# Kernel optimization log

Measured on AMD Instinct MI355X. Metric: run time of the kernel, lower is better.

## Reference

```python
import jax, jax.numpy as jnp
import numpy as np

B, N, E = 2, 4096, 256
H, TAU = 8, 32
HD = E // H
SCALING = HD ** -0.5


def setup_inputs() -> dict:
    key0 = jax.random.key(0)
    kq, kk, kv, kw = jax.random.split(key0, 4)
    return {
        "query": jax.random.normal(kq, (B, N, E), dtype=jnp.float32),
        "key": jax.random.normal(kk, (B, N, E), dtype=jnp.float32),
        "value": jax.random.normal(kv, (B, N, E), dtype=jnp.float32),
        "W": jax.random.normal(kw, (E, E), dtype=jnp.float32) * 0.02,
        "b": jnp.zeros((E,), dtype=jnp.float32),
    }


def reference(query, key, value, W, b):
    b_, n_, e_ = query.shape
    # Zero-pad the front so token i attends to keys/values at positions
    # [i - TAU + 1, ..., i] (sliding causal window of length TAU).
    pad = jnp.zeros((b_, TAU - 1, e_), dtype=query.dtype)
    kp = jnp.concatenate([pad, key], axis=1)   # [B, N+TAU-1, E]
    vp = jnp.concatenate([pad, value], axis=1)
    win_idx = jnp.arange(n_)[:, None] + jnp.arange(TAU)[None, :]  # [N, TAU]
    wk = kp[:, win_idx]  # [B, N, TAU, E] (materialized windows, as torch unfold does)
    wv = vp[:, win_idx]

    proj = lambda x: x @ W.T + b  # shared projection for q, k, v (single nn.Linear)
    q = proj(query).reshape(b_, n_, H, HD)            # [B, N, H, HD]
    k = proj(wk).reshape(b_, n_, TAU, H, HD)          # [B, N, TAU, H, HD]
    v = proj(wv).reshape(b_, n_, TAU, H, HD)

    scores = jnp.einsum("bnhd,bnthd->bhnt", q, k) * SCALING  # [B, H, N, TAU]
    attn = jax.nn.softmax(scores, axis=-1)
    out = jnp.einsum("bhnt,bnthd->bnhd", attn, v)             # [B, N, H, HD]
    return out.reshape(b_, n_, e_)
```

## Files before the change

### kernel.cpp

```cpp
#include <hip/hip_runtime.h>

#define SCALING 0.17677669529663687f

typedef __attribute__((ext_vector_type(8))) short bf8;
typedef __attribute__((ext_vector_type(4))) short bf4;
typedef _Float16 half8 __attribute__((ext_vector_type(8)));
typedef _Float16 half4 __attribute__((ext_vector_type(4)));
typedef __attribute__((ext_vector_type(4))) float floatx4;

__device__ __forceinline__ short f2bf(float f) {
    union { float f; unsigned u; } v; v.f = f;
    unsigned u = v.u;
    return (short)((u + 0x7FFFu + ((u >> 16) & 1u)) >> 16);
}

#define PSTR 264
#define VSTR 72

__global__ __launch_bounds__(512, 2) void fused_kernel(
    const float* __restrict__ q, const float* __restrict__ k,
    const float* __restrict__ v, const float* __restrict__ W,
    const float* __restrict__ bias, float* __restrict__ out)
{
    __shared__ short    Pl[96][PSTR];
    __shared__ _Float16 Vt[256][VSTR];
    __shared__ _Float16 Ps[8][32][VSTR];
    __shared__ short    As[160][40];
    __shared__ short    Bs[256][40];

    const int tid = threadIdx.x;
    const int n0  = blockIdx.x * 32;
    const int b   = blockIdx.y;
    const int lane = tid & 63, wid = tid >> 6;
    const int wm = wid & 1, wn = wid >> 1;
    const int quad = lane >> 4, l16 = lane & 15;

    int a_row[3]; int a_c4[3]; const float* a_ptr[3];
    #pragma unroll
    for (int i = 0; i < 3; i++) {
        int idx = tid + i * 512;
        if (idx < 1280) {
            int r = idx >> 3;
            a_row[i] = r;
            a_c4[i]  = (idx & 7) * 4;
            const float* p;
            if (r < 32) {
                p = q + (size_t)(b * 4096 + n0 + r) * 256;
            } else if (r < 96) {
                int j = n0 + r - 64;
                p = (j >= 0) ? (k + (size_t)(b * 4096 + j) * 256) : nullptr;
            } else {
                int j = n0 + r - 128;
                p = (j >= 0) ? (v + (size_t)(b * 4096 + j) * 256) : nullptr;
            }
            a_ptr[i] = p;
        } else { a_row[i] = -1; a_c4[i] = 0; a_ptr[i] = nullptr; }
    }
    int w_row[4], w_c4[4];
    #pragma unroll
    for (int i = 0; i < 4; i++) {
        int idx = tid + i * 512;
        w_row[i] = idx >> 3;
        w_c4[i]  = (idx & 7) * 4;
    }

    floatx4 acc[5][4];
    #pragma unroll
    for (int mt = 0; mt < 5; mt++)
        #pragma unroll
        for (int nt = 0; nt < 4; nt++) acc[mt][nt] = (floatx4)0.0f;

    for (int k0 = 0; k0 < 256; k0 += 32) {
        bf4 ab[3];
        #pragma unroll
        for (int i = 0; i < 3; i++) {
            float4 xa = make_float4(0.f, 0.f, 0.f, 0.f);
            if (a_ptr[i]) xa = *(const float4*)(a_ptr[i] + k0 + a_c4[i]);
            ab[i][0] = f2bf(xa.x); ab[i][1] = f2bf(xa.y);
            ab[i][2] = f2bf(xa.z); ab[i][3] = f2bf(xa.w);
        }
        bf4 wb[4];
        #pragma unroll
        for (int i = 0; i < 4; i++) {
            float4 wv = *(const float4*)(W + (size_t)w_row[i] * 256 + k0 + w_c4[i]);
            wb[i][0] = f2bf(wv.x); wb[i][1] = f2bf(wv.y);
            wb[i][2] = f2bf(wv.z); wb[i][3] = f2bf(wv.w);
        }
        __syncthreads();
        #pragma unroll
        for (int i = 0; i < 3; i++)
            if (a_row[i] >= 0) *(bf4*)&As[a_row[i]][a_c4[i]] = ab[i];
        #pragma unroll
        for (int i = 0; i < 4; i++)
            *(bf4*)&Bs[w_row[i]][w_c4[i]] = wb[i];
        __syncthreads();

        bf8 af[5], bfr[4];
        #pragma unroll
        for (int mt = 0; mt < 5; mt++)
            af[mt] = *(const bf8*)&As[wm * 80 + mt * 16 + l16][quad * 8];
        #pragma unroll
        for (int nt = 0; nt < 4; nt++)
            bfr[nt] = *(const bf8*)&Bs[wn * 64 + nt * 16 + l16][quad * 8];
        #pragma unroll
        for (int mt = 0; mt < 5; mt++)
            #pragma unroll
            for (int nt = 0; nt < 4; nt++)
                acc[mt][nt] = __builtin_amdgcn_mfma_f32_16x16x32_bf16(
                    af[mt], bfr[nt], acc[mt][nt], 0, 0, 0);
    }

    #pragma unroll
    for (int nt = 0; nt < 4; nt++) {
        int col = wn * 64 + nt * 16 + l16;
        float bv = bias[col];
        #pragma unroll
        for (int mt = 0; mt < 5; mt++) {
            int rb = wm * 80 + mt * 16 + quad * 4;
            if (rb < 96) {
                const bool isQ = (rb < 32);
                #pragma unroll
                for (int r = 0; r < 4; r++) {
                    float val = acc[mt][nt][r] + bv;
                    Pl[rb + r][col] = f2bf(isQ ? val * SCALING : val);
                }
            } else {
                half4 hv;
                #pragma unroll
                for (int r = 0; r < 4; r++) hv[r] = (_Float16)(acc[mt][nt][r] + bv);
                *(half4*)&Vt[col][rb - 96] = hv;
            }
        }
    }
    __syncthreads();

    const int h  = wid;
    const int cb = h * 32;

    bf8 qf[2], kf[4];
    #pragma unroll
    for (int mt = 0; mt < 2; mt++)
        qf[mt] = *(const bf8*)&Pl[mt * 16 + l16][cb + quad * 8];
    #pragma unroll
    for (int jt = 0; jt < 4; jt++)
        kf[jt] = *(const bf8*)&Pl[32 + jt * 16 + l16][cb + quad * 8];

    floatx4 S[2][4];
    S[0][0] = __builtin_amdgcn_mfma_f32_16x16x32_bf16(qf[0], kf[0], (floatx4)0.f, 0, 0, 0);
    S[0][1] = __builtin_amdgcn_mfma_f32_16x16x32_bf16(qf[0], kf[1], (floatx4)0.f, 0, 0, 0);
    S[0][2] = __builtin_amdgcn_mfma_f32_16x16x32_bf16(qf[0], kf[2], (floatx4)0.f, 0, 0, 0);
    S[1][1] = __builtin_amdgcn_mfma_f32_16x16x32_bf16(qf[1], kf[1], (floatx4)0.f, 0, 0, 0);
    S[1][2] = __builtin_amdgcn_mfma_f32_16x16x32_bf16(qf[1], kf[2], (floatx4)0.f, 0, 0, 0);
    S[1][3] = __builtin_amdgcn_mfma_f32_16x16x32_bf16(qf[1], kf[3], (floatx4)0.f, 0, 0, 0);

    float p[2][3][4], inv[2][4];
    #pragma unroll
    for (int mt = 0; mt < 2; mt++) {
        #pragma unroll
        for (int r = 0; r < 4; r++) {
            int n = mt * 16 + quad * 4 + r;
            float sv[3], mx = -3.0e38f;
            #pragma unroll
            for (int u = 0; u < 3; u++) {
                int i = (u + mt) * 16 + l16;
                bool valid = (i > n) && (i <= n + 32);
                sv[u] = valid ? S[mt][u + mt][r] : -3.0e38f;
                mx = fmaxf(mx, sv[u]);
            }
            #pragma unroll
            for (int off = 1; off < 16; off <<= 1)
                mx = fmaxf(mx, __shfl_xor(mx, off, 64));
            float lsum = 0.f;
            #pragma unroll
            for (int u = 0; u < 3; u++) {
                float pv = (sv[u] > -1.0e38f) ? __expf(sv[u] - mx) : 0.f;
                p[mt][u][r] = pv;
                lsum += pv;
            }
            #pragma unroll
            for (int off = 1; off < 16; off <<= 1)
                lsum += __shfl_xor(lsum, off, 64);
            inv[mt][r] = 1.0f / lsum;
        }
    }

    _Float16 (*myPs)[VSTR] = Ps[h];
    #pragma unroll
    for (int mt = 0; mt < 2; mt++) {
        int zjt = (mt == 0) ? 3 : 0;
        #pragma unroll
        for (int r = 0; r < 4; r++) {
            int row = mt * 16 + quad * 4 + r;
            #pragma unroll
            for (int u = 0; u < 3; u++)
                myPs[row][(u + mt) * 16 + l16] = (_Float16)p[mt][u][r];
            myPs[row][zjt * 16 + l16] = (_Float16)0.f;
        }
    }

    half8 pf[2][2], vf[2][2];
    #pragma unroll
    for (int mt = 0; mt < 2; mt++)
        #pragma unroll
        for (int ks = 0; ks < 2; ks++)
            pf[mt][ks] = *(const half8*)&myPs[mt * 16 + l16][ks * 32 + quad * 8];
    #pragma unroll
    for (int dt = 0; dt < 2; dt++)
        #pragma unroll
        for (int ks = 0; ks < 2; ks++)
            vf[dt][ks] = *(const half8*)&Vt[cb + dt * 16 + l16][ks * 32 + quad * 8];

    floatx4 O[2][2];
    #pragma unroll
    for (int mt = 0; mt < 2; mt++)
        #pragma unroll
        for (int dt = 0; dt < 2; dt++) {
            O[mt][dt] = (floatx4)0.f;
            #pragma unroll
            for (int ks = 0; ks < 2; ks++)
                O[mt][dt] = __builtin_amdgcn_mfma_f32_16x16x32_f16(
                    pf[mt][ks], vf[dt][ks], O[mt][dt], 0, 0, 0);
        }

    const size_t obase = ((size_t)b * 4096 + n0) * 256;
    #pragma unroll
    for (int mt = 0; mt < 2; mt++)
        #pragma unroll
        for (int dt = 0; dt < 2; dt++)
            #pragma unroll
            for (int r = 0; r < 4; r++) {
                int n = mt * 16 + quad * 4 + r;
                out[obase + (size_t)n * 256 + cb + dt * 16 + l16] =
                    O[mt][dt][r] * inv[mt][r];
            }
}

extern "C" void kernel_launch(void* const* d_in, const int* in_sizes, int n_in,
                              void* d_out, int out_size, void* d_ws, size_t ws_size,
                              hipStream_t stream) {
    (void)in_sizes; (void)n_in; (void)out_size; (void)d_ws; (void)ws_size;
    const float* q    = (const float*)d_in[0];
    const float* k    = (const float*)d_in[1];
    const float* v    = (const float*)d_in[2];
    const float* W    = (const float*)d_in[3];
    const float* bias = (const float*)d_in[4];
    float* outp = (float*)d_out;

    hipLaunchKernelGGL(fused_kernel, dim3(128, 2), dim3(512), 0, stream,
                       q, k, v, W, bias, outp);
}
```

Before: 92.42 us.

## Pre-convert W to bf16, double-buffer A tiles, load W fragments from global

Adds a small pre-kernel that converts W to bf16 once per call in workspace. The main kernel now reads W fragments straight from global memory into registers, dropping the Bs shared tile. It double-buffers the activation tile with register prefetch so only one barrier is needed per k-step, and uses the hardware v_cvt_pk_bf16_f32 instruction instead of manual rounding. It also swizzles the block index to change the order in which sequence chunks are scheduled. The costs are an extra kernel launch and uncoalesced per-lane global reads of W.

```diff
diff --git a/kernel.cpp b/kernel.cpp
--- a/kernel.cpp
+++ b/kernel.cpp
@@ -8,28 +8,44 @@
 typedef _Float16 half4 __attribute__((ext_vector_type(4)));
 typedef __attribute__((ext_vector_type(4))) float floatx4;
 
-__device__ __forceinline__ short f2bf(float f) {
-    union { float f; unsigned u; } v; v.f = f;
-    unsigned u = v.u;
-    return (short)((u + 0x7FFFu + ((u >> 16) & 1u)) >> 16);
+__device__ __forceinline__ int cvt_pk_bf16(float a, float b) {
+    int r;
+    asm("v_cvt_pk_bf16_f32 %0, %1, %2" : "=v"(r) : "v"(a), "v"(b));
+    return r;
+}
+__device__ __forceinline__ bf4 cvt4_bf(float4 x) {
+    union { int i[2]; bf4 v; } u;
+    u.i[0] = cvt_pk_bf16(x.x, x.y);
+    u.i[1] = cvt_pk_bf16(x.z, x.w);
+    return u.v;
+}
+__device__ __forceinline__ short f2bf_hw(float f) {
+    return (short)cvt_pk_bf16(f, f);
 }
 
 #define PSTR 264
 #define VSTR 72
 
+__global__ void prep_w_kernel(const float* __restrict__ W, short* __restrict__ Wb) {
+    int i = (blockIdx.x * 256 + threadIdx.x) * 4;
+    float4 w = *(const float4*)(W + i);
+    *(bf4*)(Wb + i) = cvt4_bf(w);
+}
+
 __global__ __launch_bounds__(512, 2) void fused_kernel(
     const float* __restrict__ q, const float* __restrict__ k,
-    const float* __restrict__ v, const float* __restrict__ W,
+    const float* __restrict__ v, const short* __restrict__ Wb,
     const float* __restrict__ bias, float* __restrict__ out)
 {
     __shared__ short    Pl[96][PSTR];
     __shared__ _Float16 Vt[256][VSTR];
     __shared__ _Float16 Ps[8][32][VSTR];
-    __shared__ short    As[160][40];
-    __shared__ short    Bs[256][40];
+    __shared__ short    As[2][160][40];
 
     const int tid = threadIdx.x;
-    const int n0  = blockIdx.x * 32;
+    const int bxr = blockIdx.x;
+    const int bx  = (bxr & 7) * 16 + (bxr >> 3);
+    const int n0  = bx * 32;
     const int b   = blockIdx.y;
     const int lane = tid & 63, wid = tid >> 6;
     const int wm = wid & 1, wn = wid >> 1;
@@ -56,13 +72,11 @@
             a_ptr[i] = p;
         } else { a_row[i] = -1; a_c4[i] = 0; a_ptr[i] = nullptr; }
     }
-    int w_row[4], w_c4[4];
-    #pragma unroll
-    for (int i = 0; i < 4; i++) {
-        int idx = tid + i * 512;
-        w_row[i] = idx >> 3;
-        w_c4[i]  = (idx & 7) * 4;
-    }
+
+    const short* wfp[4];
+    #pragma unroll
+    for (int nt = 0; nt < 4; nt++)
+        wfp[nt] = Wb + (size_t)(wn * 64 + nt * 16 + l16) * 256 + quad * 8;
 
     floatx4 acc[5][4];
     #pragma unroll
@@ -70,44 +84,61 @@
         #pragma unroll
         for (int nt = 0; nt < 4; nt++) acc[mt][nt] = (floatx4)0.0f;
 
-    for (int k0 = 0; k0 < 256; k0 += 32) {
-        bf4 ab[3];
-        #pragma unroll
-        for (int i = 0; i < 3; i++) {
-            float4 xa = make_float4(0.f, 0.f, 0.f, 0.f);
-            if (a_ptr[i]) xa = *(const float4*)(a_ptr[i] + k0 + a_c4[i]);
-            ab[i][0] = f2bf(xa.x); ab[i][1] = f2bf(xa.y);
-            ab[i][2] = f2bf(xa.z); ab[i][3] = f2bf(xa.w);
-        }
-        bf4 wb[4];
-        #pragma unroll
-        for (int i = 0; i < 4; i++) {
-            float4 wv = *(const float4*)(W + (size_t)w_row[i] * 256 + k0 + w_c4[i]);
-            wb[i][0] = f2bf(wv.x); wb[i][1] = f2bf(wv.y);
-            wb[i][2] = f2bf(wv.z); wb[i][3] = f2bf(wv.w);
-        }
+    float4 xain[3];
+    #pragma unroll
+    for (int i = 0; i < 3; i++) {
+        xain[i] = make_float4(0.f, 0.f, 0.f, 0.f);
+        if (a_ptr[i]) xain[i] = *(const float4*)(a_ptr[i] + a_c4[i]);
+    }
+    #pragma unroll
+    for (int i = 0; i < 3; i++) {
+        bf4 t = cvt4_bf(xain[i]);
+        if (a_row[i] >= 0) *(bf4*)&As[0][a_row[i]][a_c4[i]] = t;
+    }
+    #pragma unroll
+    for (int i = 0; i < 3; i++) {
+        float4 t = make_float4(0.f, 0.f, 0.f, 0.f);
+        if (a_ptr[i]) t = *(const float4*)(a_ptr[i] + 32 + a_c4[i]);
+        xain[i] = t;
+    }
+    bf8 wf_cur[4], wf_nxt[4];
+    #pragma unroll
+    for (int nt = 0; nt < 4; nt++)
+        wf_cur[nt] = *(const bf8*)(wfp[nt]);
+
+    for (int it = 0; it < 8; ++it) {
+        const int cur = it & 1;
         __syncthreads();
-        #pragma unroll
-        for (int i = 0; i < 3; i++)
-            if (a_row[i] >= 0) *(bf4*)&As[a_row[i]][a_c4[i]] = ab[i];
-        #pragma unroll
-        for (int i = 0; i < 4; i++)
-            *(bf4*)&Bs[w_row[i]][w_c4[i]] = wb[i];
-        __syncthreads();
-
-        bf8 af[5], bfr[4];
+        bf8 af[5];
         #pragma unroll
         for (int mt = 0; mt < 5; mt++)
-            af[mt] = *(const bf8*)&As[wm * 80 + mt * 16 + l16][quad * 8];
-        #pragma unroll
-        for (int nt = 0; nt < 4; nt++)
-            bfr[nt] = *(const bf8*)&Bs[wn * 64 + nt * 16 + l16][quad * 8];
+            af[mt] = *(const bf8*)&As[cur][wm * 80 + mt * 16 + l16][quad * 8];
+        if (it < 7) {
+            #pragma unroll
+            for (int i = 0; i < 3; i++) {
+                bf4 t = cvt4_bf(xain[i]);
+                if (a_row[i] >= 0) *(bf4*)&As[cur ^ 1][a_row[i]][a_c4[i]] = t;
+            }
+            #pragma unroll
+            for (int nt = 0; nt < 4; nt++)
+                wf_nxt[nt] = *(const bf8*)(wfp[nt] + (it + 1) * 32);
+        }
+        if (it < 6) {
+            #pragma unroll
+            for (int i = 0; i < 3; i++) {
+                float4 t = make_float4(0.f, 0.f, 0.f, 0.f);
+                if (a_ptr[i]) t = *(const float4*)(a_ptr[i] + (it + 2) * 32 + a_c4[i]);
+                xain[i] = t;
+            }
+        }
         #pragma unroll
         for (int mt = 0; mt < 5; mt++)
             #pragma unroll
             for (int nt = 0; nt < 4; nt++)
                 acc[mt][nt] = __builtin_amdgcn_mfma_f32_16x16x32_bf16(
-                    af[mt], bfr[nt], acc[mt][nt], 0, 0, 0);
+                    af[mt], wf_cur[nt], acc[mt][nt], 0, 0, 0);
+        #pragma unroll
+        for (int nt = 0; nt < 4; nt++) wf_cur[nt] = wf_nxt[nt];
     }
 
     #pragma unroll
@@ -122,7 +153,7 @@
                 #pragma unroll
                 for (int r = 0; r < 4; r++) {
                     float val = acc[mt][nt][r] + bv;
-                    Pl[rb + r][col] = f2bf(isQ ? val * SCALING : val);
+                    Pl[rb + r][col] = f2bf_hw(isQ ? val * SCALING : val);
                 }
             } else {
                 half4 hv;
@@ -238,14 +269,16 @@
 extern "C" void kernel_launch(void* const* d_in, const int* in_sizes, int n_in,
                               void* d_out, int out_size, void* d_ws, size_t ws_size,
                               hipStream_t stream) {
-    (void)in_sizes; (void)n_in; (void)out_size; (void)d_ws; (void)ws_size;
+    (void)in_sizes; (void)n_in; (void)out_size; (void)ws_size;
     const float* q    = (const float*)d_in[0];
     const float* k    = (const float*)d_in[1];
     const float* v    = (const float*)d_in[2];
     const float* W    = (const float*)d_in[3];
     const float* bias = (const float*)d_in[4];
     float* outp = (float*)d_out;
-
+    short* Wb   = (short*)d_ws;
+
+    hipLaunchKernelGGL(prep_w_kernel, dim3(64), dim3(256), 0, stream, W, Wb);
     hipLaunchKernelGGL(fused_kernel, dim3(128, 2), dim3(512), 0, stream,
-                       q, k, v, W, bias, outp);
-}
+                       q, k, v, Wb, bias, outp);
+}
```

Measured after the change: 91.30 us. No clear change (-1.2%).
